# Kernel tuning notes

Measured on AMD Instinct MI355X. Metric: run time of the kernel, lower is better.

Reference implementation:

```python
import jax, jax.numpy as jnp
import numpy as np

LN_EPS = 1e-5

def _layer_norm(x, gamma, beta):
    mu = jnp.mean(x, axis=-1, keepdims=True)
    var = jnp.mean(jnp.square(x - mu), axis=-1, keepdims=True)
    return (x - mu) * jax.lax.rsqrt(var + LN_EPS) * gamma + beta

def setup_inputs() -> dict:
    key = jax.random.key(0)
    ks = jax.random.split(key, 10)
    B, S, D_IN = 8, 2048, 1024
    H1, H2, C = 2048, 1024, 64
    s1 = 1.0 / np.sqrt(D_IN)
    s2 = 1.0 / np.sqrt(H1)
    s3 = 1.0 / np.sqrt(H2)
    return {
        "embeddings": jax.random.normal(ks[0], (B, S, D_IN), jnp.float32),
        "prior_evidence": jax.random.normal(ks[1], (B, C), jnp.float32),
        "W1": jax.random.uniform(ks[2], (D_IN, H1), jnp.float32, -s1, s1),
        "b1": jnp.zeros((H1,), jnp.float32),
        "g1": jnp.ones((H1,), jnp.float32),
        "beta1": jnp.zeros((H1,), jnp.float32),
        "W2": jax.random.uniform(ks[3], (H1, H2), jnp.float32, -s2, s2),
        "b2": jnp.zeros((H2,), jnp.float32),
        "g2": jnp.ones((H2,), jnp.float32),
        "beta2": jnp.zeros((H2,), jnp.float32),
        "Wh": jax.random.uniform(ks[4], (H2, C), jnp.float32, -s3, s3),
        "bh": jnp.zeros((C,), jnp.float32),
        "and_gate": jnp.ones((C,), jnp.float32),
        "or_gate": jnp.ones((C,), jnp.float32),
    }

def reference(embeddings, prior_evidence, W1, b1, g1, beta1, W2, b2, g2, beta2, Wh, bh, and_gate, or_gate):
    # feature extractor: Linear -> ReLU -> Dropout(eval: identity) -> LayerNorm, x2
    h = _layer_norm(jax.nn.relu(embeddings @ W1 + b1), g1, beta1)
    features = _layer_norm(jax.nn.relu(h @ W2 + b2), g2, beta2)  # [B,S,H2]
    d = features.shape[-1]
    scores = jnp.einsum('bsd,btd->bst', features, features) / jnp.sqrt(jnp.float32(d))
    attention_weights = jax.nn.softmax(scores, axis=-1)          # [B,S,S]
    attended = jnp.einsum('bst,btd->bsd', attention_weights, features)
    logits = attended @ Wh + bh                                   # [B,S,C]
    sig_l = jax.nn.sigmoid(logits)
    sig_p = jax.nn.sigmoid(prior_evidence)[:, None, :]            # [B,1,C] broadcasts
    and_ev = jnp.minimum(sig_l, sig_p) * and_gate
    or_ev = jnp.maximum(sig_l, sig_p) * or_gate
    logits = jnp.log((and_ev + or_ev) / 2 + 1e-10)
    return (logits, attention_weights)
```

## Files before the change

### kernel.cpp

```cpp
#include <hip/hip_runtime.h>

typedef unsigned short u16;
typedef __bf16 bf16x8 __attribute__((ext_vector_type(8)));
typedef float f32x4 __attribute__((ext_vector_type(4)));

__device__ __forceinline__ u16 f2bf(float f) {
    unsigned u = __float_as_uint(f);
    u = (u + 0x7FFFu + ((u >> 16) & 1u)) >> 16;
    return (u16)u;
}
__device__ __forceinline__ float bf2f(u16 h) {
    return __uint_as_float(((unsigned)h) << 16);
}

__device__ __forceinline__ void gld16(const u16* g, u16* l) {
    __builtin_amdgcn_global_load_lds((const __attribute__((address_space(1))) void*)g,
                                     (__attribute__((address_space(3))) void*)l, 16, 0, 0);
}

__device__ __forceinline__ int swz(int row, int col) {
    return ((row >> 4) * 2 + (col >> 5)) * 512 + (row & 15) * 32 +
           ((col & 31) ^ ((row & 8) ? 16 : 0));
}

__global__ __launch_bounds__(256) void cvt_kernel(const float* __restrict__ in,
                                                  u16* __restrict__ out, long n) {
    long i = ((long)blockIdx.x * blockDim.x + threadIdx.x) * 4;
    if (i + 3 < n) {
        float4 v = *(const float4*)&in[i];
        __align__(8) u16 r[4] = {f2bf(v.x), f2bf(v.y), f2bf(v.z), f2bf(v.w)};
        *(int2*)&out[i] = *(const int2*)r;
    }
}

template <int INF32>
__global__ __launch_bounds__(256) void transpose_to_bf16(const void* __restrict__ in,
                                                         u16* __restrict__ out, int R, int C,
                                                         long inB, long outB) {
    __shared__ float tile[32][33];
    const long zi = (long)blockIdx.z * inB;
    const long zo = (long)blockIdx.z * outB;
    const int c0 = blockIdx.x * 32, r0 = blockIdx.y * 32;
    const int tx = threadIdx.x & 31;
    const int ty = threadIdx.x >> 5;
#pragma unroll
    for (int i = 0; i < 32; i += 8) {
        long idx = zi + (long)(r0 + ty + i) * C + c0 + tx;
        float v = INF32 ? ((const float*)in)[idx] : bf2f(((const u16*)in)[idx]);
        tile[ty + i][tx] = v;
    }
    __syncthreads();
#pragma unroll
    for (int i = 0; i < 32; i += 8) {
        out[zo + (long)(c0 + ty + i) * R + r0 + tx] = f2bf(tile[tx][ty + i]);
    }
}

template <int OUTBF>
__global__ __launch_bounds__(512, 2) void gemm_nt(const u16* __restrict__ A,
                                                  const u16* __restrict__ Bm,
                                                  void* __restrict__ Cout, int M, int N, int K,
                                                  long sA, long sB, long sC,
                                                  const float* __restrict__ bias, int act,
                                                  float scale, int symm,
                                                  const float* __restrict__ rscale) {
    int bx, by, zz;
    if (symm) {
        const int q = gridDim.x >> 3;
        const int orig = blockIdx.x;
        const int wgid = (orig & 7) * q + (orig >> 3);
        const int NB = N >> 8;
        const int nTri = (NB * (NB + 1)) >> 1;
        zz = wgid / nTri;
        int t = wgid - zz * nTri;
        by = 0;
        int rem = NB;
        while (t >= rem) {
            t -= rem;
            --rem;
            ++by;
        }
        bx = by + t;
    } else {
        const int nx = gridDim.x;
        const int nwg = nx * gridDim.y;
        const int orig = blockIdx.y * nx + blockIdx.x;
        const int q = nwg >> 3, r = nwg & 7, xcd = orig & 7, o8 = orig >> 3;
        const int wgid = (xcd < r ? xcd * (q + 1) : r * (q + 1) + (xcd - r) * q) + o8;
        bx = wgid % nx;
        by = wgid / nx;
        zz = blockIdx.z;
    }

    __shared__ __align__(16) u16 As[2][256 * 64];
    __shared__ __align__(16) u16 Bs[2][256 * 64];
    const int tid = threadIdx.x;
    const int lane = tid & 63;
    const int wid = tid >> 6;
    const int wr = wid >> 2;
    const int wc = wid & 3;
    const int l15 = lane & 15, lg = lane >> 4;
    const long zA = (long)zz * sA;
    const long zB = (long)zz * sB;
    const long zC = (long)zz * sC;
    const int m0 = by * 256, n0 = bx * 256;
    const u16* Ab = A + zA + (long)m0 * K;
    const u16* Bb = Bm + zB + (long)n0 * K;
    const int nt = K >> 6;

    f32x4 acc[8][4] = {};

    auto stage_chunk = [&](int t, int b, int j) {
        const int c = j * 512 + tid;
        const int s = c >> 6, r = (c >> 2) & 15;
        const int row = (s >> 1) * 16 + r;
        const int col = (s & 1) * 32 + (((c & 3) * 8) ^ ((r & 8) ? 16 : 0));
        gld16(Ab + (long)row * K + t * 64 + col, &As[b][c * 8]);
        gld16(Bb + (long)row * K + t * 64 + col, &Bs[b][c * 8]);
    };

#pragma unroll
    for (int j = 0; j < 4; ++j) stage_chunk(0, 0, j);
    if (nt > 1) {
        stage_chunk(1, 1, 0);
        asm volatile("s_waitcnt vmcnt(2)" ::: "memory");
    } else {
        asm volatile("s_waitcnt vmcnt(0)" ::: "memory");
    }
    __builtin_amdgcn_s_barrier();

    for (int t = 0; t < nt; ++t) {
        const int cur = t & 1;
        bf16x8 bf[4][2];
#pragma unroll
        for (int n = 0; n < 4; ++n)
#pragma unroll
            for (int kk = 0; kk < 2; ++kk)
                bf[n][kk] = *(const bf16x8*)&Bs[cur][swz(wc * 64 + n * 16 + l15, kk * 32 + lg * 8)];
        bf16x8 af[2][2][2];
#pragma unroll
        for (int mi = 0; mi < 2; ++mi)
#pragma unroll
            for (int kk = 0; kk < 2; ++kk)
                af[0][mi][kk] =
                    *(const bf16x8*)&As[cur][swz(wr * 128 + mi * 16 + l15, kk * 32 + lg * 8)];
#pragma unroll
        for (int mg = 0; mg < 4; ++mg) {
            if (mg < 3) {
#pragma unroll
                for (int mi = 0; mi < 2; ++mi)
#pragma unroll
                    for (int kk = 0; kk < 2; ++kk)
                        af[(mg + 1) & 1][mi][kk] = *(const bf16x8*)&As[cur][swz(
                            wr * 128 + (mg + 1) * 32 + mi * 16 + l15, kk * 32 + lg * 8)];
                if (t + 1 < nt) stage_chunk(t + 1, cur ^ 1, mg + 1);
            }
            __builtin_amdgcn_s_setprio(1);
#pragma unroll
            for (int mi = 0; mi < 2; ++mi)
#pragma unroll
                for (int n = 0; n < 4; ++n)
#pragma unroll
                    for (int kk = 0; kk < 2; ++kk)
                        acc[mg * 2 + mi][n] = __builtin_amdgcn_mfma_f32_16x16x32_bf16(
                            af[mg & 1][mi][kk], bf[n][kk], acc[mg * 2 + mi][n], 0, 0, 0);
            __builtin_amdgcn_s_setprio(0);
        }
        __builtin_amdgcn_s_barrier();
        if (t + 2 < nt) {
            stage_chunk(t + 2, cur, 0);
            asm volatile("s_waitcnt vmcnt(2)" ::: "memory");
        } else {
            asm volatile("s_waitcnt vmcnt(0)" ::: "memory");
        }
        __builtin_amdgcn_s_barrier();
    }

#pragma unroll
    for (int n = 0; n < 4; ++n) {
        const int col = n0 + wc * 64 + n * 16 + l15;
        const float bv = bias ? bias[col] : 0.0f;
#pragma unroll
        for (int m = 0; m < 8; ++m) {
            const int rowb = m0 + wr * 128 + m * 16 + lg * 4;
            float v[4];
#pragma unroll
            for (int r = 0; r < 4; ++r) {
                float f = acc[m][n][r] * scale + bv;
                if (act == 1)
                    f = fmaxf(f, 0.0f);
                else if (act == 2)
                    f = __expf(f - 32.0f);
                if (rscale) f *= rscale[(long)zz * M + rowb + r];
                v[r] = f;
                if (OUTBF)
                    ((u16*)Cout)[zC + (long)(rowb + r) * N + col] = f2bf(f);
                else
                    ((float*)Cout)[zC + (long)(rowb + r) * N + col] = f;
            }
            if (symm && bx > by) {
                if (OUTBF) {
                    __align__(8) u16 tv[4] = {f2bf(v[0]), f2bf(v[1]), f2bf(v[2]), f2bf(v[3])};
                    *(int2*)&((u16*)Cout)[zC + (long)col * N + rowb] = *(const int2*)tv;
                } else {
                    *(float4*)&((float*)Cout)[zC + (long)col * N + rowb] =
                        make_float4(v[0], v[1], v[2], v[3]);
                }
            }
        }
    }
}

template <int CH>
__global__ __launch_bounds__(256) void ln_wave(u16* __restrict__ x, const float* __restrict__ g,
                                               const float* __restrict__ be) {
    const int lane = threadIdx.x & 63;
    const int wid = threadIdx.x >> 6;
    const long row = (long)blockIdx.x * 4 + wid;
    u16* p = x + row * (CH * 512);
    __align__(16) u16 raw[CH][8];
    float s = 0.f, ss = 0.f;
#pragma unroll
    for (int c = 0; c < CH; ++c) {
        *(int4*)raw[c] = *(const int4*)&p[(c * 64 + lane) * 8];
#pragma unroll
        for (int j = 0; j < 8; ++j) {
            float f = bf2f(raw[c][j]);
            s += f;
            ss += f * f;
        }
    }
#pragma unroll
    for (int o = 1; o < 64; o <<= 1) {
        s += __shfl_xor(s, o);
        ss += __shfl_xor(ss, o);
    }
    const float inv = 1.0f / (float)(CH * 512);
    const float mu = s * inv;
    const float var = ss * inv - mu * mu;
    const float rs = rsqrtf(var + 1e-5f);
#pragma unroll
    for (int c = 0; c < CH; ++c) {
        const int base = (c * 64 + lane) * 8;
        float4 g0 = *(const float4*)&g[base];
        float4 g1 = *(const float4*)&g[base + 4];
        float4 b0 = *(const float4*)&be[base];
        float4 b1 = *(const float4*)&be[base + 4];
        float gv[8] = {g0.x, g0.y, g0.z, g0.w, g1.x, g1.y, g1.z, g1.w};
        float bv[8] = {b0.x, b0.y, b0.z, b0.w, b1.x, b1.y, b1.z, b1.w};
#pragma unroll
        for (int j = 0; j < 8; ++j)
            raw[c][j] = f2bf((bf2f(raw[c][j]) - mu) * rs * gv[j] + bv[j]);
        *(int4*)&p[base] = *(const int4*)raw[c];
    }
}

__global__ __launch_bounds__(256) void norm_wave(const u16* __restrict__ e,
                                                 float* __restrict__ outw,
                                                 float* __restrict__ rowInv) {
    const int lane = threadIdx.x & 63;
    const int wid = threadIdx.x >> 6;
    const long row = (long)blockIdx.x * 4 + wid;
    const u16* p = e + row * 2048;
    float v[4][8];
    float s = 0.f;
#pragma unroll
    for (int c = 0; c < 4; ++c) {
        __align__(16) u16 raw[8];
        *(int4*)raw = *(const int4*)&p[(c * 64 + lane) * 8];
#pragma unroll
        for (int j = 0; j < 8; ++j) {
            v[c][j] = bf2f(raw[j]);
            s += v[c][j];
        }
    }
#pragma unroll
    for (int o = 1; o < 64; o <<= 1) s += __shfl_xor(s, o);
    const float inv = 1.0f / s;
    if (lane == 0) rowInv[row] = inv;
    float* q = outw + row * 2048;
#pragma unroll
    for (int c = 0; c < 4; ++c) {
        const int base = (c * 64 + lane) * 8;
        float4 o0 = make_float4(v[c][0] * inv, v[c][1] * inv, v[c][2] * inv, v[c][3] * inv);
        float4 o1 = make_float4(v[c][4] * inv, v[c][5] * inv, v[c][6] * inv, v[c][7] * inv);
        *(float4*)&q[base] = o0;
        *(float4*)&q[base + 4] = o1;
    }
}

__global__ __launch_bounds__(256) void head_kernel(const u16* __restrict__ A,
                                                   const u16* __restrict__ WhT,
                                                   const float* __restrict__ bh,
                                                   const float* __restrict__ prior,
                                                   const float* __restrict__ ag,
                                                   const float* __restrict__ og,
                                                   float* __restrict__ out) {
    __shared__ __align__(16) u16 As2[128 * 64];
    __shared__ __align__(16) u16 Bs2[64 * 64];
    const int tid = threadIdx.x;
    const int lane = tid & 63;
    const int wid = tid >> 6;
    const int l15 = lane & 15, lg = lane >> 4;
    const int m0 = blockIdx.x * 128;
    const int srow = tid >> 3, scol = (tid & 7) * 8;
    const u16* pa = A + (long)(m0 + srow) * 1024 + scol;
    const u16* pb = WhT + (long)srow * 1024 + scol;

    f32x4 acc[2][4] = {};
    for (int k0 = 0; k0 < 1024; k0 += 64) {
#pragma unroll
        for (int i = 0; i < 4; ++i) gld16(pa + (long)i * 32 * 1024 + k0, &As2[i * 2048 + tid * 8]);
#pragma unroll
        for (int i = 0; i < 2; ++i) gld16(pb + (long)i * 32 * 1024 + k0, &Bs2[i * 2048 + tid * 8]);
        __syncthreads();
#pragma unroll
        for (int kk = 0; kk < 2; ++kk) {
            bf16x8 af[2], bfr[4];
#pragma unroll
            for (int m = 0; m < 2; ++m)
                af[m] = *(const bf16x8*)&As2[(wid * 32 + m * 16 + l15) * 64 + kk * 32 + lg * 8];
#pragma unroll
            for (int n = 0; n < 4; ++n)
                bfr[n] = *(const bf16x8*)&Bs2[(n * 16 + l15) * 64 + kk * 32 + lg * 8];
#pragma unroll
            for (int m = 0; m < 2; ++m)
#pragma unroll
                for (int n = 0; n < 4; ++n)
                    acc[m][n] =
                        __builtin_amdgcn_mfma_f32_16x16x32_bf16(af[m], bfr[n], acc[m][n], 0, 0, 0);
        }
        __syncthreads();
    }

#pragma unroll
    for (int n = 0; n < 4; ++n) {
        const int col = n * 16 + l15;
        const float bhv = bh[col];
        const float agv = ag[col];
        const float ogv = og[col];
#pragma unroll
        for (int m = 0; m < 2; ++m) {
#pragma unroll
            for (int r = 0; r < 4; ++r) {
                const int row = m0 + wid * 32 + m * 16 + lg * 4 + r;
                const float logit = acc[m][n][r] + bhv;
                const int b = row >> 11;
                const float sp = 1.f / (1.f + expf(-prior[b * 64 + col]));
                const float sl = 1.f / (1.f + expf(-logit));
                const float av = fminf(sl, sp) * agv;
                const float ov = fmaxf(sl, sp) * ogv;
                out[(long)row * 64 + col] = logf((av + ov) * 0.5f + 1e-10f);
            }
        }
    }
}

extern "C" void kernel_launch(void* const* d_in, const int* in_sizes, int n_in, void* d_out,
                              int out_size, void* d_ws, size_t ws_size, hipStream_t stream) {
    const float* emb = (const float*)d_in[0];
    const float* prior = (const float*)d_in[1];
    const float* W1 = (const float*)d_in[2];
    const float* b1 = (const float*)d_in[3];
    const float* g1 = (const float*)d_in[4];
    const float* be1 = (const float*)d_in[5];
    const float* W2 = (const float*)d_in[6];
    const float* b2 = (const float*)d_in[7];
    const float* g2 = (const float*)d_in[8];
    const float* be2 = (const float*)d_in[9];
    const float* Wh = (const float*)d_in[10];
    const float* bh = (const float*)d_in[11];
    const float* ag = (const float*)d_in[12];
    const float* og = (const float*)d_in[13];

    const int Bn = 8, S = 2048, DIN = 1024, H1 = 2048, H2 = 1024, Cc = 64;
    const int M = Bn * S;

    char* ws = (char*)d_ws;
    size_t off = 0;
    auto alloc = [&](size_t b) {
        size_t o = off;
        off += (b + 255) & ~(size_t)255;
        return o;
    };
    char* R0 = ws + alloc((size_t)M * H1 * 2);
    char* R1 = ws + alloc((size_t)M * DIN * 2);
    char* R2 = ws + alloc((size_t)M * H2 * 2);
    u16* W1t = (u16*)(ws + alloc((size_t)H1 * DIN * 2));
    u16* W2t = (u16*)(ws + alloc((size_t)H2 * H1 * 2));
    u16* WhT = (u16*)(ws + alloc((size_t)Cc * H2 * 2));
    float* rowInv = (float*)(ws + alloc((size_t)M * 4));

    u16* h = (u16*)R0;
    u16* attnb = (u16*)R0;
    u16* embb = (u16*)R1;
    u16* featT = (u16*)R1;
    u16* feat = (u16*)R2;
    u16* attd = (u16*)R2;

    float* out_logits = (float*)d_out;
    float* out_attn = out_logits + (size_t)M * Cc;

    cvt_kernel<<<(int)(((long)M * DIN) / 1024), 256, 0, stream>>>(emb, embb, (long)M * DIN);
    transpose_to_bf16<1><<<dim3(H1 / 32, DIN / 32, 1), 256, 0, stream>>>(W1, W1t, DIN, H1, 0, 0);
    transpose_to_bf16<1><<<dim3(H2 / 32, H1 / 32, 1), 256, 0, stream>>>(W2, W2t, H1, H2, 0, 0);
    transpose_to_bf16<1><<<dim3(Cc / 32, H2 / 32, 1), 256, 0, stream>>>(Wh, WhT, H2, Cc, 0, 0);
    gemm_nt<1><<<dim3(H1 / 256, M / 256, 1), 512, 0, stream>>>(embb, W1t, h, M, H1, DIN, 0, 0, 0,
                                                               b1, 1, 1.0f, 0, nullptr);
    ln_wave<4><<<M / 4, 256, 0, stream>>>(h, g1, be1);
    gemm_nt<1><<<dim3(H2 / 256, M / 256, 1), 512, 0, stream>>>(h, W2t, feat, M, H2, H1, 0, 0, 0,
                                                               b2, 1, 1.0f, 0, nullptr);
    ln_wave<2><<<M / 4, 256, 0, stream>>>(feat, g2, be2);
    transpose_to_bf16<0><<<dim3(H2 / 32, S / 32, Bn), 256, 0, stream>>>(
        feat, featT, S, H2, (long)S * H2, (long)H2 * S);
    {
        const int NB = S / 256;
        const int nTri = NB * (NB + 1) / 2;
        gemm_nt<1><<<dim3(nTri * Bn, 1, 1), 512, 0, stream>>>(
            feat, feat, attnb, S, S, H2, (long)S * H2, (long)S * H2, (long)S * S, nullptr,
            2, 0.03125f, 1, nullptr);
    }
    norm_wave<<<M / 4, 256, 0, stream>>>(attnb, out_attn, rowInv);
    gemm_nt<1><<<dim3(H2 / 256, S / 256, Bn), 512, 0, stream>>>(attnb, featT, attd, S, H2, S,
                                                                (long)S * S, (long)H2 * S,
                                                                (long)S * H2, nullptr, 0, 1.0f, 0,
                                                                rowInv);
    head_kernel<<<M / 128, 256, 0, stream>>>(attd, WhT, bh, prior, ag, og, out_logits);
}
```

Measured before the change: 467.5 us.

## Shrink GEMM tiles to 128x128x32 with simpler double-buffered pipeline

The GEMM kernel moves from 256x256 tiles with K=64 steps, 512 threads and a finely interleaved staging schedule to 128x128 tiles with K=32 steps and 256 threads. It uses a new XOR swizzle and a plain prefetch-next-tile loop that drains all loads each iteration. This cuts per-block LDS and register use so more blocks fit per CU and more tiles are available. In exchange, operand reuse per tile drops, global traffic rises, and the per-iteration full vmcnt wait with small K steps may expose memory latency.

```diff
diff --git a/kernel.cpp b/kernel.cpp
--- a/kernel.cpp
+++ b/kernel.cpp
@@ -16,11 +16,6 @@
 __device__ __forceinline__ void gld16(const u16* g, u16* l) {
     __builtin_amdgcn_global_load_lds((const __attribute__((address_space(1))) void*)g,
                                      (__attribute__((address_space(3))) void*)l, 16, 0, 0);
-}
-
-__device__ __forceinline__ int swz(int row, int col) {
-    return ((row >> 4) * 2 + (col >> 5)) * 512 + (row & 15) * 32 +
-           ((col & 31) ^ ((row & 8) ? 16 : 0));
 }
 
 __global__ __launch_bounds__(256) void cvt_kernel(const float* __restrict__ in,
@@ -57,7 +52,7 @@
 }
 
 template <int OUTBF>
-__global__ __launch_bounds__(512, 2) void gemm_nt(const u16* __restrict__ A,
+__global__ __launch_bounds__(256, 3) void gemm_nt(const u16* __restrict__ A,
                                                   const u16* __restrict__ Bm,
                                                   void* __restrict__ Cout, int M, int N, int K,
                                                   long sA, long sB, long sC,
@@ -69,7 +64,7 @@
         const int q = gridDim.x >> 3;
         const int orig = blockIdx.x;
         const int wgid = (orig & 7) * q + (orig >> 3);
-        const int NB = N >> 8;
+        const int NB = N >> 7;
         const int nTri = (NB * (NB + 1)) >> 1;
         zz = wgid / nTri;
         int t = wgid - zz * nTri;
@@ -92,87 +87,61 @@
         zz = blockIdx.z;
     }
 
-    __shared__ __align__(16) u16 As[2][256 * 64];
-    __shared__ __align__(16) u16 Bs[2][256 * 64];
+    __shared__ __align__(16) u16 As[2][128 * 32];
+    __shared__ __align__(16) u16 Bs[2][128 * 32];
     const int tid = threadIdx.x;
     const int lane = tid & 63;
     const int wid = tid >> 6;
-    const int wr = wid >> 2;
-    const int wc = wid & 3;
+    const int wr = wid >> 1;
+    const int wc = wid & 1;
     const int l15 = lane & 15, lg = lane >> 4;
     const long zA = (long)zz * sA;
     const long zB = (long)zz * sB;
     const long zC = (long)zz * sC;
-    const int m0 = by * 256, n0 = bx * 256;
+    const int m0 = by * 128, n0 = bx * 128;
     const u16* Ab = A + zA + (long)m0 * K;
     const u16* Bb = Bm + zB + (long)n0 * K;
-    const int nt = K >> 6;
-
-    f32x4 acc[8][4] = {};
-
-    auto stage_chunk = [&](int t, int b, int j) {
-        const int c = j * 512 + tid;
-        const int s = c >> 6, r = (c >> 2) & 15;
-        const int row = (s >> 1) * 16 + r;
-        const int col = (s & 1) * 32 + (((c & 3) * 8) ^ ((r & 8) ? 16 : 0));
-        gld16(Ab + (long)row * K + t * 64 + col, &As[b][c * 8]);
-        gld16(Bb + (long)row * K + t * 64 + col, &Bs[b][c * 8]);
+    const int nt = K >> 5;
+
+    f32x4 acc[4][4] = {};
+
+    auto stage = [&](int x, int b) {
+#pragma unroll
+        for (int j = 0; j < 2; ++j) {
+            const int c = j * 256 + tid;
+            const int row = c >> 2;
+            const int col = (((c & 3) ^ ((row >> 1) & 3)) << 3);
+            gld16(Ab + (long)row * K + x * 32 + col, &As[b][c * 8]);
+            gld16(Bb + (long)row * K + x * 32 + col, &Bs[b][c * 8]);
+        }
     };
 
-#pragma unroll
-    for (int j = 0; j < 4; ++j) stage_chunk(0, 0, j);
-    if (nt > 1) {
-        stage_chunk(1, 1, 0);
-        asm volatile("s_waitcnt vmcnt(2)" ::: "memory");
-    } else {
-        asm volatile("s_waitcnt vmcnt(0)" ::: "memory");
-    }
+    stage(0, 0);
+    asm volatile("s_waitcnt vmcnt(0)" ::: "memory");
     __builtin_amdgcn_s_barrier();
+
+    const int sx = (l15 >> 1) & 3;
+    const int go = ((lg ^ sx) << 3) + (l15 & 1) * 0;
 
     for (int t = 0; t < nt; ++t) {
         const int cur = t & 1;
-        bf16x8 bf[4][2];
+        if (t + 1 < nt) stage(t + 1, cur ^ 1);
+        bf16x8 af[4], bf[4];
 #pragma unroll
         for (int n = 0; n < 4; ++n)
-#pragma unroll
-            for (int kk = 0; kk < 2; ++kk)
-                bf[n][kk] = *(const bf16x8*)&Bs[cur][swz(wc * 64 + n * 16 + l15, kk * 32 + lg * 8)];
-        bf16x8 af[2][2][2];
-#pragma unroll
-        for (int mi = 0; mi < 2; ++mi)
-#pragma unroll
-            for (int kk = 0; kk < 2; ++kk)
-                af[0][mi][kk] =
-                    *(const bf16x8*)&As[cur][swz(wr * 128 + mi * 16 + l15, kk * 32 + lg * 8)];
-#pragma unroll
-        for (int mg = 0; mg < 4; ++mg) {
-            if (mg < 3) {
-#pragma unroll
-                for (int mi = 0; mi < 2; ++mi)
-#pragma unroll
-                    for (int kk = 0; kk < 2; ++kk)
-                        af[(mg + 1) & 1][mi][kk] = *(const bf16x8*)&As[cur][swz(
-                            wr * 128 + (mg + 1) * 32 + mi * 16 + l15, kk * 32 + lg * 8)];
-                if (t + 1 < nt) stage_chunk(t + 1, cur ^ 1, mg + 1);
-            }
-            __builtin_amdgcn_s_setprio(1);
-#pragma unroll
-            for (int mi = 0; mi < 2; ++mi)
-#pragma unroll
-                for (int n = 0; n < 4; ++n)
-#pragma unroll
-                    for (int kk = 0; kk < 2; ++kk)
-                        acc[mg * 2 + mi][n] = __builtin_amdgcn_mfma_f32_16x16x32_bf16(
-                            af[mg & 1][mi][kk], bf[n][kk], acc[mg * 2 + mi][n], 0, 0, 0);
-            __builtin_amdgcn_s_setprio(0);
-        }
-        __builtin_amdgcn_s_barrier();
-        if (t + 2 < nt) {
-            stage_chunk(t + 2, cur, 0);
-            asm volatile("s_waitcnt vmcnt(2)" ::: "memory");
-        } else {
-            asm volatile("s_waitcnt vmcnt(0)" ::: "memory");
-        }
+            bf[n] = *(const bf16x8*)&Bs[cur][(wc * 64 + n * 16 + l15) * 32 + go];
+#pragma unroll
+        for (int m = 0; m < 4; ++m)
+            af[m] = *(const bf16x8*)&As[cur][(wr * 64 + m * 16 + l15) * 32 + go];
+        __builtin_amdgcn_s_setprio(1);
+#pragma unroll
+        for (int m = 0; m < 4; ++m)
+#pragma unroll
+            for (int n = 0; n < 4; ++n)
+                acc[m][n] =
+                    __builtin_amdgcn_mfma_f32_16x16x32_bf16(af[m], bf[n], acc[m][n], 0, 0, 0);
+        __builtin_amdgcn_s_setprio(0);
+        asm volatile("s_waitcnt vmcnt(0)" ::: "memory");
         __builtin_amdgcn_s_barrier();
     }
 
@@ -181,8 +150,8 @@
         const int col = n0 + wc * 64 + n * 16 + l15;
         const float bv = bias ? bias[col] : 0.0f;
 #pragma unroll
-        for (int m = 0; m < 8; ++m) {
-            const int rowb = m0 + wr * 128 + m * 16 + lg * 4;
+        for (int m = 0; m < 4; ++m) {
+            const int rowb = m0 + wr * 64 + m * 16 + lg * 4;
             float v[4];
 #pragma unroll
             for (int r = 0; r < 4; ++r) {
@@ -405,23 +374,23 @@
     transpose_to_bf16<1><<<dim3(H1 / 32, DIN / 32, 1), 256, 0, stream>>>(W1, W1t, DIN, H1, 0, 0);
     transpose_to_bf16<1><<<dim3(H2 / 32, H1 / 32, 1), 256, 0, stream>>>(W2, W2t, H1, H2, 0, 0);
     transpose_to_bf16<1><<<dim3(Cc / 32, H2 / 32, 1), 256, 0, stream>>>(Wh, WhT, H2, Cc, 0, 0);
-    gemm_nt<1><<<dim3(H1 / 256, M / 256, 1), 512, 0, stream>>>(embb, W1t, h, M, H1, DIN, 0, 0, 0,
+    gemm_nt<1><<<dim3(H1 / 128, M / 128, 1), 256, 0, stream>>>(embb, W1t, h, M, H1, DIN, 0, 0, 0,
                                                                b1, 1, 1.0f, 0, nullptr);
     ln_wave<4><<<M / 4, 256, 0, stream>>>(h, g1, be1);
-    gemm_nt<1><<<dim3(H2 / 256, M / 256, 1), 512, 0, stream>>>(h, W2t, feat, M, H2, H1, 0, 0, 0,
+    gemm_nt<1><<<dim3(H2 / 128, M / 128, 1), 256, 0, stream>>>(h, W2t, feat, M, H2, H1, 0, 0, 0,
                                                                b2, 1, 1.0f, 0, nullptr);
     ln_wave<2><<<M / 4, 256, 0, stream>>>(feat, g2, be2);
     transpose_to_bf16<0><<<dim3(H2 / 32, S / 32, Bn), 256, 0, stream>>>(
         feat, featT, S, H2, (long)S * H2, (long)H2 * S);
     {
-        const int NB = S / 256;
+        const int NB = S / 128;
         const int nTri = NB * (NB + 1) / 2;
-        gemm_nt<1><<<dim3(nTri * Bn, 1, 1), 512, 0, stream>>>(
+        gemm_nt<1><<<dim3(nTri * Bn, 1, 1), 256, 0, stream>>>(
             feat, feat, attnb, S, S, H2, (long)S * H2, (long)S * H2, (long)S * S, nullptr,
             2, 0.03125f, 1, nullptr);
     }
     norm_wave<<<M / 4, 256, 0, stream>>>(attnb, out_attn, rowInv);
-    gemm_nt<1><<<dim3(H2 / 256, S / 256, Bn), 512, 0, stream>>>(attnb, featT, attd, S, H2, S,
+    gemm_nt<1><<<dim3(H2 / 128, S / 128, Bn), 256, 0, stream>>>(attnb, featT, attd, S, H2, S,
                                                                 (long)S * S, (long)H2 * S,
                                                                 (long)S * H2, nullptr, 0, 1.0f, 0,
                                                                 rowInv);
```

After: 481.1 us. 2.9% more time.

## Stage mirrored symmetric tile through LDS and remap tiles per XCD

Applied to the files above, without the earlier changes.

For symmetric GEMM tiles with bf16 output, the transposed copy is written into a padded shared-memory buffer and then stored to global memory as coalesced 16-byte rows, replacing scattered 8-byte column writes. The XCD-aware tile mapping is also changed so each XCD covers a contiguous band of rows, column-major within the band, to improve L2 reuse. The combined shared-memory buffer is enlarged to hold the transpose tile. This adds a barrier and extra LDS traffic in the epilogue.

```diff
diff --git a/kernel.cpp b/kernel.cpp
--- a/kernel.cpp
+++ b/kernel.cpp
@@ -87,13 +87,22 @@
         const int orig = blockIdx.y * nx + blockIdx.x;
         const int q = nwg >> 3, r = nwg & 7, xcd = orig & 7, o8 = orig >> 3;
         const int wgid = (xcd < r ? xcd * (q + 1) : r * (q + 1) + (xcd - r) * q) + o8;
-        bx = wgid % nx;
-        by = wgid / nx;
+        if (r == 0 && (q % nx) == 0) {
+            const int rpc = q / nx;
+            const int o = wgid - xcd * q;
+            by = xcd * rpc + (o % rpc);
+            bx = o / rpc;
+        } else {
+            bx = wgid % nx;
+            by = wgid / nx;
+        }
         zz = blockIdx.z;
     }
 
-    __shared__ __align__(16) u16 As[2][256 * 64];
-    __shared__ __align__(16) u16 Bs[2][256 * 64];
+    __shared__ __align__(16) u16 SM[67584];
+    u16(*As)[256 * 64] = (u16(*)[256 * 64])SM;
+    u16(*Bs)[256 * 64] = (u16(*)[256 * 64])(SM + 32768);
+    u16* T = SM;
     const int tid = threadIdx.x;
     const int lane = tid & 63;
     const int wid = tid >> 6;
@@ -176,6 +185,7 @@
         __builtin_amdgcn_s_barrier();
     }
 
+    const int mirror = symm && (bx > by);
 #pragma unroll
     for (int n = 0; n < 4; ++n) {
         const int col = n0 + wc * 64 + n * 16 + l15;
@@ -198,15 +208,27 @@
                 else
                     ((float*)Cout)[zC + (long)(rowb + r) * N + col] = f;
             }
-            if (symm && bx > by) {
+            if (mirror) {
                 if (OUTBF) {
+                    const int cl = wc * 64 + n * 16 + l15;
+                    const int rl = wr * 128 + m * 16 + lg * 4;
                     __align__(8) u16 tv[4] = {f2bf(v[0]), f2bf(v[1]), f2bf(v[2]), f2bf(v[3])};
-                    *(int2*)&((u16*)Cout)[zC + (long)col * N + rowb] = *(const int2*)tv;
+                    *(int2*)&T[cl * 264 + rl] = *(const int2*)tv;
                 } else {
                     *(float4*)&((float*)Cout)[zC + (long)col * N + rowb] =
                         make_float4(v[0], v[1], v[2], v[3]);
                 }
             }
+        }
+    }
+    if (mirror && OUTBF) {
+        __builtin_amdgcn_s_barrier();
+#pragma unroll
+        for (int i = 0; i < 16; ++i) {
+            const int c = i * 512 + tid;
+            const int tr = c >> 5, tc = c & 31;
+            *(int4*)&((u16*)Cout)[zC + (long)(n0 + tr) * N + m0 + tc * 8] =
+                *(const int4*)&T[tr * 264 + tc * 8];
         }
     }
 }
```

Result: faster. 451.9 us, median of 7 (-3.3%).
